# Performance work log

Hardware: AMD Instinct MI355X
Metric: run time of the kernel (lower is better)

The kernel has to match this reference:

```python
import jax, jax.numpy as jnp
import numpy as np

N_NODES = 50000
N_EDGES = 500000
F_IN = 16      # node feature dim F
F_OUT = 16     # channels F_
E_FEAT = 8     # edge feature dim
HIDDEN = 32    # kernel_network hidden size


def _glorot(key, shape):
    fan_in, fan_out = shape[0], shape[1]
    lim = np.sqrt(6.0 / (fan_in + fan_out)).astype(np.float32)
    return jax.random.uniform(key, shape, jnp.float32, -lim, lim)


def setup_inputs() -> dict:
    key = jax.random.key(0)
    ks = jax.random.split(key, 8)
    x = jax.random.normal(ks[0], (N_NODES, F_IN), jnp.float32)
    e = jax.random.uniform(ks[1], (N_EDGES, E_FEAT), jnp.float32)
    idx_i = jax.random.randint(ks[2], (N_EDGES,), 0, N_NODES, jnp.int32)  # targets
    idx_j = jax.random.randint(ks[3], (N_EDGES,), 0, N_NODES, jnp.int32)  # sources
    W1 = _glorot(ks[4], (E_FEAT, HIDDEN))
    b1 = jnp.zeros((HIDDEN,), jnp.float32)
    W2 = _glorot(ks[5], (HIDDEN, F_OUT * F_IN))
    b2 = jnp.zeros((F_OUT * F_IN,), jnp.float32)
    root_kernel = _glorot(ks[6], (F_IN, F_OUT))
    bias = jnp.zeros((F_OUT,), jnp.float32)
    return {"x": x, "e": e, "idx_i": idx_i, "idx_j": idx_j,
            "W1": W1, "b1": b1, "W2": W2, "b2": b2,
            "root_kernel": root_kernel, "bias": bias}


def reference(x, e, idx_i, idx_j, W1, b1, W2, b2, root_kernel, bias):
    # Edge-conditioned filter-generating network (MLP, relu hidden, linear out)
    h = jax.nn.relu(e @ W1 + b1)                       # [E, HIDDEN]
    kern = (h @ W2 + b2).reshape(-1, F_IN, F_OUT)      # [E, F, F_]
    # gather source node features, per-edge matmul, scatter-add to targets
    msg = jnp.einsum('ef,efc->ec', x[idx_j], kern)     # [E, F_]
    out = jax.ops.segment_sum(msg, idx_i, num_segments=N_NODES)  # [N, F_]
    out = out + x @ root_kernel + bias
    return out
```

## Files before the change

kernel.cpp:

```cpp
#include <hip/hip_runtime.h>

typedef __attribute__((ext_vector_type(8))) short bf16x8_t;
typedef __attribute__((ext_vector_type(4))) float f32x4_t;

__device__ __forceinline__ unsigned short f2bf(float f) {
    union { float f; unsigned int i; } v; v.f = f;
    unsigned int u = v.i;
    return (unsigned short)((u + 0x7FFFu + ((u >> 16) & 1u)) >> 16);
}

__device__ __forceinline__ unsigned int cvt_pk_bf16(float lo, float hi) {
    unsigned int r;
    asm("v_cvt_pk_bf16_f32 %0, %1, %2" : "=v"(r) : "v"(lo), "v"(hi));
    return r;
}

#define LD4(p) (*reinterpret_cast<const float4*>(p))


__global__ __launch_bounds__(256) void prep_kernel(
    const float* __restrict__ x,
    const float* __restrict__ W1,
    const float* __restrict__ b1,
    const float* __restrict__ W2,
    const float* __restrict__ b2,
    const float* __restrict__ rootk,
    const float* __restrict__ bias,
    float* __restrict__ out,
    unsigned short* __restrict__ tab,
    int n_nodes, int root_blocks)
{
    const int tid = threadIdx.x;
    const int bid = blockIdx.x;

    if (bid < root_blocks) {
        __shared__ float sR[256];
        __shared__ float sB[16];
        if (tid < 256) sR[tid] = rootk[tid];
        if (tid < 16)  sB[tid] = bias[tid];
        __syncthreads();

        int nid = bid * 256 + tid;
        if (nid >= n_nodes) return;

        const float* xp = x + (size_t)nid * 16;
        float xf[16];
#pragma unroll
        for (int f = 0; f < 16; f += 4) {
            float4 v = LD4(xp + f);
            xf[f] = v.x; xf[f + 1] = v.y; xf[f + 2] = v.z; xf[f + 3] = v.w;
        }
        float o[16];
#pragma unroll
        for (int cc = 0; cc < 16; ++cc) o[cc] = sB[cc];
#pragma unroll
        for (int f = 0; f < 16; ++f) {
            float p = xf[f];
#pragma unroll
            for (int cc = 0; cc < 16; ++cc)
                o[cc] = fmaf(p, sR[f * 16 + cc], o[cc]);
        }
        float* dst = out + (size_t)nid * 16;
#pragma unroll
        for (int cc = 0; cc < 16; cc += 4)
            *reinterpret_cast<float4*>(dst + cc) = make_float4(o[cc], o[cc+1], o[cc+2], o[cc+3]);
    } else {
        for (int it = tid; it < 64 * 19; it += 256) {
            int grp  = it >> 6;
            int lane = it & 63;
            int q = lane >> 4, cc = lane & 15;
            union { unsigned short h[8]; uint4 u; } pk;
            if (grp < 2) {
                int hh = grp;
#pragma unroll
                for (int j = 0; j < 8; ++j) {
                    float v = 0.f;
                    if (q == 0)              v = W1[j * 32 + cc + 16 * hh];
                    else if (q == 1 && j==0) v = b1[cc + 16 * hh];
                    pk.h[j] = f2bf(v);
                }
                *reinterpret_cast<uint4*>(tab + ((size_t)hh * 64 + lane) * 8) = pk.u;
            } else {
                int s = grp - 2;
#pragma unroll
                for (int j = 0; j < 8; ++j) {
                    float v;
                    if (s < 16) {
                        int hd = (j < 4) ? (4 * q + j) : (4 * q + 12 + j);
                        v = W2[hd * 256 + s * 16 + cc];
                    } else {
                        v = (q < 2) ? b2[(q * 8 + j) * 16 + cc] : 0.f;
                    }
                    pk.h[j] = f2bf(v);
                }
                *reinterpret_cast<uint4*>(tab + 1024 + ((size_t)s * 64 + lane) * 8) = pk.u;
            }
        }
    }
}

template<int EXACT>
__global__ __launch_bounds__(256) void edge_mfma_kernel(
    const float* __restrict__ x,
    const float* __restrict__ efeat,
    const int*   __restrict__ idx_i,
    const int*   __restrict__ idx_j,
    const unsigned short* __restrict__ tab,
    float* __restrict__ out,
    int n_edges, int n_groups)
{
    const int lane = threadIdx.x & 63;
    const int q = lane >> 4;
    const int c = lane & 15;

    const bf16x8_t* w1f = reinterpret_cast<const bf16x8_t*>(tab) + lane;
    const bf16x8_t aW1_0 = w1f[0];
    const bf16x8_t aW1_1 = w1f[64];
    const bf16x8_t* w2f = reinterpret_cast<const bf16x8_t*>(tab + 1024) + lane;
    bf16x8_t bW2[17];
#pragma unroll
    for (int s = 0; s < 17; ++s) bW2[s] = w2f[s * 64];

    const unsigned int c1 = (q == 1) ? 0x00003F80u : 0u;
    const bool isq0 = (q == 0);
    const bool qodd = (q & 1);
    float* const outc = out + c;

    const int wid = blockIdx.x * 4 + (threadIdx.x >> 6);
    const int g0  = wid * 4;
    if (g0 >= n_groups) return;
    const int rem = n_groups - g0;

    auto ldj = [&](int gg) -> int {
        int eid = gg * 16 + c;
        if (!EXACT) { if (eid >= n_edges) eid = n_edges - 1; }
        return idx_j[eid];
    };
    auto eoff = [&](int gg) -> size_t {
        int eid = gg * 16 + c;
        if (!EXACT) { if (eid >= n_edges) eid = n_edges - 1; }
        return (size_t)eid * 8;
    };

    auto compute = [&](float4 X0, float4 X1, float4 X2, float4 X3,
                       float4 E0, float4 E1, int gg) {
        int t0, t1, t2, t3;
        if (EXACT || (gg * 16 + 16 <= n_edges)) {
            int4 tv = *reinterpret_cast<const int4*>(idx_i + gg * 16 + q * 4);
            t0 = tv.x; t1 = tv.y; t2 = tv.z; t3 = tv.w;
        } else {
            const int eb = gg * 16 + q * 4;
            t0 = (eb + 0 < n_edges) ? idx_i[eb + 0] : 0;
            t1 = (eb + 1 < n_edges) ? idx_i[eb + 1] : 0;
            t2 = (eb + 2 < n_edges) ? idx_i[eb + 2] : 0;
            t3 = (eb + 3 < n_edges) ? idx_i[eb + 3] : 0;
        }

        union { bf16x8_t bf; unsigned int u[4]; } bB;
        {
            unsigned int ef0 = cvt_pk_bf16(E0.x, E0.y);
            unsigned int ef1 = cvt_pk_bf16(E0.z, E0.w);
            unsigned int ef2 = cvt_pk_bf16(E1.x, E1.y);
            unsigned int ef3 = cvt_pk_bf16(E1.z, E1.w);
            bB.u[0] = isq0 ? ef0 : c1;
            bB.u[1] = isq0 ? ef1 : 0u;
            bB.u[2] = isq0 ? ef2 : 0u;
            bB.u[3] = isq0 ? ef3 : 0u;
        }
        f32x4_t z4 = {0.f, 0.f, 0.f, 0.f};
        f32x4_t h0 = __builtin_amdgcn_mfma_f32_16x16x32_bf16(aW1_0, bB.bf, z4, 0, 0, 0);
        f32x4_t h1 = __builtin_amdgcn_mfma_f32_16x16x32_bf16(aW1_1, bB.bf, z4, 0, 0, 0);

        float hown[8];
#pragma unroll
        for (int r = 0; r < 4; ++r) {
            hown[r]     = fmaxf(h0[r], 0.f);
            hown[4 + r] = fmaxf(h1[r], 0.f);
        }

        float xf[16];
        xf[0]=X0.x; xf[1]=X0.y; xf[2]=X0.z; xf[3]=X0.w;
        xf[4]=X1.x; xf[5]=X1.y; xf[6]=X1.z; xf[7]=X1.w;
        xf[8]=X2.x; xf[9]=X2.y; xf[10]=X2.z; xf[11]=X2.w;
        xf[12]=X3.x; xf[13]=X3.y; xf[14]=X3.z; xf[15]=X3.w;

        union { bf16x8_t bf; unsigned int u[4]; } xb;
        xb.u[0] = cvt_pk_bf16(qodd ? xf[8]  : xf[0], qodd ? xf[9]  : xf[1]);
        xb.u[1] = cvt_pk_bf16(qodd ? xf[10] : xf[2], qodd ? xf[11] : xf[3]);
        xb.u[2] = cvt_pk_bf16(qodd ? xf[12] : xf[4], qodd ? xf[13] : xf[5]);
        xb.u[3] = cvt_pk_bf16(qodd ? xf[14] : xf[6], qodd ? xf[15] : xf[7]);

        f32x4_t acc0 = {0.f, 0.f, 0.f, 0.f};
        f32x4_t acc1 = {0.f, 0.f, 0.f, 0.f};
        union { bf16x8_t bf; unsigned int u[4]; } afr;
#pragma unroll
        for (int s = 0; s < 16; s += 2) {
            float xs = xf[s];
            afr.u[0] = cvt_pk_bf16(hown[0] * xs, hown[1] * xs);
            afr.u[1] = cvt_pk_bf16(hown[2] * xs, hown[3] * xs);
            afr.u[2] = cvt_pk_bf16(hown[4] * xs, hown[5] * xs);
            afr.u[3] = cvt_pk_bf16(hown[6] * xs, hown[7] * xs);
            acc0 = __builtin_amdgcn_mfma_f32_16x16x32_bf16(afr.bf, bW2[s], acc0, 0, 0, 0);
            xs = xf[s + 1];
            afr.u[0] = cvt_pk_bf16(hown[0] * xs, hown[1] * xs);
            afr.u[1] = cvt_pk_bf16(hown[2] * xs, hown[3] * xs);
            afr.u[2] = cvt_pk_bf16(hown[4] * xs, hown[5] * xs);
            afr.u[3] = cvt_pk_bf16(hown[6] * xs, hown[7] * xs);
            acc1 = __builtin_amdgcn_mfma_f32_16x16x32_bf16(afr.bf, bW2[s + 1], acc1, 0, 0, 0);
        }
        acc0 = __builtin_amdgcn_mfma_f32_16x16x32_bf16(xb.bf, bW2[16], acc0, 0, 0, 0);

        const float rr0 = acc0[0] + acc1[0];
        const float rr1 = acc0[1] + acc1[1];
        const float rr2 = acc0[2] + acc1[2];
        const float rr3 = acc0[3] + acc1[3];
        if (EXACT) {
            atomicAdd(outc + (size_t)t0 * 16, rr0);
            atomicAdd(outc + (size_t)t1 * 16, rr1);
            atomicAdd(outc + (size_t)t2 * 16, rr2);
            atomicAdd(outc + (size_t)t3 * 16, rr3);
        } else {
            const int eb = gg * 16 + q * 4;
            if (eb + 0 < n_edges) atomicAdd(outc + (size_t)t0 * 16, rr0);
            if (eb + 1 < n_edges) atomicAdd(outc + (size_t)t1 * 16, rr1);
            if (eb + 2 < n_edges) atomicAdd(outc + (size_t)t2 * 16, rr2);
            if (eb + 3 < n_edges) atomicAdd(outc + (size_t)t3 * 16, rr3);
        }
    };

#define STAGE(B0,B1,B2,B3,BE0,BE1, jv, gg)                         \
    {                                                              \
        const float* xp = x + (size_t)(jv) * 16;                   \
        B0 = LD4(xp); B1 = LD4(xp + 4);                            \
        B2 = LD4(xp + 8); B3 = LD4(xp + 12);                       \
        const float* ep = efeat + eoff(gg);                        \
        BE0 = LD4(ep); BE1 = LD4(ep + 4);                          \
    }

    const int jA = ldj(g0);
    const int jB = (rem > 1) ? ldj(g0 + 1) : 0;
    const int jC = (rem > 2) ? ldj(g0 + 2) : 0;
    const int jD = (rem > 3) ? ldj(g0 + 3) : 0;

    float4 a0, a1, a2, a3, ae0, ae1;
    float4 b0, b1, b2, b3, be0, be1;

    STAGE(a0,a1,a2,a3,ae0,ae1, jA, g0);
    if (rem > 1) STAGE(b0,b1,b2,b3,be0,be1, jB, g0 + 1);
    compute(a0,a1,a2,a3,ae0,ae1, g0);
    if (rem > 1) {
        if (rem > 2) STAGE(a0,a1,a2,a3,ae0,ae1, jC, g0 + 2);
        compute(b0,b1,b2,b3,be0,be1, g0 + 1);
        if (rem > 2) {
            if (rem > 3) STAGE(b0,b1,b2,b3,be0,be1, jD, g0 + 3);
            compute(a0,a1,a2,a3,ae0,ae1, g0 + 2);
            if (rem > 3) compute(b0,b1,b2,b3,be0,be1, g0 + 3);
        }
    }
#undef STAGE
}

extern "C" void kernel_launch(void* const* d_in, const int* in_sizes, int n_in,
                              void* d_out, int out_size, void* d_ws, size_t ws_size,
                              hipStream_t stream) {
    const float* x     = (const float*)d_in[0];
    const float* e     = (const float*)d_in[1];
    const int*   idx_i = (const int*)d_in[2];
    const int*   idx_j = (const int*)d_in[3];
    const float* W1    = (const float*)d_in[4];
    const float* b1    = (const float*)d_in[5];
    const float* W2    = (const float*)d_in[6];
    const float* b2    = (const float*)d_in[7];
    const float* rootk = (const float*)d_in[8];
    const float* bias  = (const float*)d_in[9];

    int n_nodes  = in_sizes[0] / 16;
    int n_edges  = in_sizes[2];
    int n_groups = (n_edges + 15) / 16;

    float* out = (float*)d_out;
    unsigned short* tab = (unsigned short*)d_ws;

    int root_blocks = (n_nodes + 255) / 256;
    prep_kernel<<<root_blocks + 1, 256, 0, stream>>>(x, W1, b1, W2, b2, rootk, bias,
                                                     out, tab, n_nodes, root_blocks);

    int blocks = (n_groups + 15) / 16;
    if ((n_edges & 15) == 0)
        edge_mfma_kernel<1><<<blocks, 256, 0, stream>>>(x, e, idx_i, idx_j, tab, out,
                                                        n_edges, n_groups);
    else
        edge_mfma_kernel<0><<<blocks, 256, 0, stream>>>(x, e, idx_i, idx_j, tab, out,
                                                        n_edges, n_groups);
}
```

Measured before the change: 44.23 us.

## Process eight edge groups per wave with triple-buffered gather prefetch

Each wave now handles eight 16-edge groups instead of four. All idx_j values are loaded up front, and a three-stage rotating register buffer keeps two gathers in flight while one group is computed. It also sets launch_bounds minimum occupancy to 2 and rewrites the hidden-times-x products as packed float2 multiplies so the compiler can emit packed FMA. The intent is to hide gather latency and amortise W2 register loading across more groups, at the cost of higher register pressure and fewer, larger waves.

```diff
diff --git a/kernel.cpp b/kernel.cpp
--- a/kernel.cpp
+++ b/kernel.cpp
@@ -2,6 +2,7 @@
 
 typedef __attribute__((ext_vector_type(8))) short bf16x8_t;
 typedef __attribute__((ext_vector_type(4))) float f32x4_t;
+typedef __attribute__((ext_vector_type(2))) float f32x2_t;
 
 __device__ __forceinline__ unsigned short f2bf(float f) {
     union { float f; unsigned int i; } v; v.f = f;
@@ -100,7 +101,7 @@
 }
 
 template<int EXACT>
-__global__ __launch_bounds__(256) void edge_mfma_kernel(
+__global__ __launch_bounds__(256, 2) void edge_mfma_kernel(
     const float* __restrict__ x,
     const float* __restrict__ efeat,
     const int*   __restrict__ idx_i,
@@ -127,19 +128,41 @@
     float* const outc = out + c;
 
     const int wid = blockIdx.x * 4 + (threadIdx.x >> 6);
-    const int g0  = wid * 4;
+    const int g0  = wid * 8;
     if (g0 >= n_groups) return;
     const int rem = n_groups - g0;
 
-    auto ldj = [&](int gg) -> int {
+    const int* jp = idx_j + (size_t)g0 * 16 + c;
+    int j0, j1, j2, j3, j4, j5, j6, j7;
+    if (EXACT) {
+        j0 = jp[0];
+        j1 = (rem > 1) ? jp[16]  : 0;
+        j2 = (rem > 2) ? jp[32]  : 0;
+        j3 = (rem > 3) ? jp[48]  : 0;
+        j4 = (rem > 4) ? jp[64]  : 0;
+        j5 = (rem > 5) ? jp[80]  : 0;
+        j6 = (rem > 6) ? jp[96]  : 0;
+        j7 = (rem > 7) ? jp[112] : 0;
+    } else {
+        auto ldj = [&](int k) -> int {
+            int eid = (g0 + k) * 16 + c;
+            if (eid >= n_edges) eid = n_edges - 1;
+            return idx_j[eid];
+        };
+        j0 = ldj(0);
+        j1 = (rem > 1) ? ldj(1) : 0;
+        j2 = (rem > 2) ? ldj(2) : 0;
+        j3 = (rem > 3) ? ldj(3) : 0;
+        j4 = (rem > 4) ? ldj(4) : 0;
+        j5 = (rem > 5) ? ldj(5) : 0;
+        j6 = (rem > 6) ? ldj(6) : 0;
+        j7 = (rem > 7) ? ldj(7) : 0;
+    }
+
+    auto eptr = [&](int gg) -> const float* {
         int eid = gg * 16 + c;
         if (!EXACT) { if (eid >= n_edges) eid = n_edges - 1; }
-        return idx_j[eid];
-    };
-    auto eoff = [&](int gg) -> size_t {
-        int eid = gg * 16 + c;
-        if (!EXACT) { if (eid >= n_edges) eid = n_edges - 1; }
-        return (size_t)eid * 8;
+        return efeat + (size_t)eid * 8;
     };
 
     auto compute = [&](float4 X0, float4 X1, float4 X2, float4 X3,
@@ -157,26 +180,20 @@
         }
 
         union { bf16x8_t bf; unsigned int u[4]; } bB;
-        {
-            unsigned int ef0 = cvt_pk_bf16(E0.x, E0.y);
-            unsigned int ef1 = cvt_pk_bf16(E0.z, E0.w);
-            unsigned int ef2 = cvt_pk_bf16(E1.x, E1.y);
-            unsigned int ef3 = cvt_pk_bf16(E1.z, E1.w);
-            bB.u[0] = isq0 ? ef0 : c1;
-            bB.u[1] = isq0 ? ef1 : 0u;
-            bB.u[2] = isq0 ? ef2 : 0u;
-            bB.u[3] = isq0 ? ef3 : 0u;
-        }
+        bB.u[0] = isq0 ? cvt_pk_bf16(E0.x, E0.y) : c1;
+        bB.u[1] = isq0 ? cvt_pk_bf16(E0.z, E0.w) : 0u;
+        bB.u[2] = isq0 ? cvt_pk_bf16(E1.x, E1.y) : 0u;
+        bB.u[3] = isq0 ? cvt_pk_bf16(E1.z, E1.w) : 0u;
+
         f32x4_t z4 = {0.f, 0.f, 0.f, 0.f};
         f32x4_t h0 = __builtin_amdgcn_mfma_f32_16x16x32_bf16(aW1_0, bB.bf, z4, 0, 0, 0);
         f32x4_t h1 = __builtin_amdgcn_mfma_f32_16x16x32_bf16(aW1_1, bB.bf, z4, 0, 0, 0);
 
-        float hown[8];
-#pragma unroll
-        for (int r = 0; r < 4; ++r) {
-            hown[r]     = fmaxf(h0[r], 0.f);
-            hown[4 + r] = fmaxf(h1[r], 0.f);
-        }
+        f32x2_t hp0, hp1, hp2, hp3;
+        hp0[0] = fmaxf(h0[0], 0.f); hp0[1] = fmaxf(h0[1], 0.f);
+        hp1[0] = fmaxf(h0[2], 0.f); hp1[1] = fmaxf(h0[3], 0.f);
+        hp2[0] = fmaxf(h1[0], 0.f); hp2[1] = fmaxf(h1[1], 0.f);
+        hp3[0] = fmaxf(h1[2], 0.f); hp3[1] = fmaxf(h1[3], 0.f);
 
         float xf[16];
         xf[0]=X0.x; xf[1]=X0.y; xf[2]=X0.z; xf[3]=X0.w;
@@ -195,17 +212,19 @@
         union { bf16x8_t bf; unsigned int u[4]; } afr;
 #pragma unroll
         for (int s = 0; s < 16; s += 2) {
-            float xs = xf[s];
-            afr.u[0] = cvt_pk_bf16(hown[0] * xs, hown[1] * xs);
-            afr.u[1] = cvt_pk_bf16(hown[2] * xs, hown[3] * xs);
-            afr.u[2] = cvt_pk_bf16(hown[4] * xs, hown[5] * xs);
-            afr.u[3] = cvt_pk_bf16(hown[6] * xs, hown[7] * xs);
+            f32x2_t xs2; xs2[0] = xf[s]; xs2[1] = xf[s];
+            f32x2_t p0 = hp0 * xs2, p1 = hp1 * xs2, p2 = hp2 * xs2, p3 = hp3 * xs2;
+            afr.u[0] = cvt_pk_bf16(p0[0], p0[1]);
+            afr.u[1] = cvt_pk_bf16(p1[0], p1[1]);
+            afr.u[2] = cvt_pk_bf16(p2[0], p2[1]);
+            afr.u[3] = cvt_pk_bf16(p3[0], p3[1]);
             acc0 = __builtin_amdgcn_mfma_f32_16x16x32_bf16(afr.bf, bW2[s], acc0, 0, 0, 0);
-            xs = xf[s + 1];
-            afr.u[0] = cvt_pk_bf16(hown[0] * xs, hown[1] * xs);
-            afr.u[1] = cvt_pk_bf16(hown[2] * xs, hown[3] * xs);
-            afr.u[2] = cvt_pk_bf16(hown[4] * xs, hown[5] * xs);
-            afr.u[3] = cvt_pk_bf16(hown[6] * xs, hown[7] * xs);
+            xs2[0] = xf[s + 1]; xs2[1] = xf[s + 1];
+            p0 = hp0 * xs2; p1 = hp1 * xs2; p2 = hp2 * xs2; p3 = hp3 * xs2;
+            afr.u[0] = cvt_pk_bf16(p0[0], p0[1]);
+            afr.u[1] = cvt_pk_bf16(p1[0], p1[1]);
+            afr.u[2] = cvt_pk_bf16(p2[0], p2[1]);
+            afr.u[3] = cvt_pk_bf16(p3[0], p3[1]);
             acc1 = __builtin_amdgcn_mfma_f32_16x16x32_bf16(afr.bf, bW2[s + 1], acc1, 0, 0, 0);
         }
         acc0 = __builtin_amdgcn_mfma_f32_16x16x32_bf16(xb.bf, bW2[16], acc0, 0, 0, 0);
@@ -233,30 +252,31 @@
         const float* xp = x + (size_t)(jv) * 16;                   \
         B0 = LD4(xp); B1 = LD4(xp + 4);                            \
         B2 = LD4(xp + 8); B3 = LD4(xp + 12);                       \
-        const float* ep = efeat + eoff(gg);                        \
+        const float* ep = eptr(gg);                                \
         BE0 = LD4(ep); BE1 = LD4(ep + 4);                          \
     }
 
-    const int jA = ldj(g0);
-    const int jB = (rem > 1) ? ldj(g0 + 1) : 0;
-    const int jC = (rem > 2) ? ldj(g0 + 2) : 0;
-    const int jD = (rem > 3) ? ldj(g0 + 3) : 0;
-
-    float4 a0, a1, a2, a3, ae0, ae1;
-    float4 b0, b1, b2, b3, be0, be1;
-
-    STAGE(a0,a1,a2,a3,ae0,ae1, jA, g0);
-    if (rem > 1) STAGE(b0,b1,b2,b3,be0,be1, jB, g0 + 1);
-    compute(a0,a1,a2,a3,ae0,ae1, g0);
-    if (rem > 1) {
-        if (rem > 2) STAGE(a0,a1,a2,a3,ae0,ae1, jC, g0 + 2);
-        compute(b0,b1,b2,b3,be0,be1, g0 + 1);
-        if (rem > 2) {
-            if (rem > 3) STAGE(b0,b1,b2,b3,be0,be1, jD, g0 + 3);
-            compute(a0,a1,a2,a3,ae0,ae1, g0 + 2);
-            if (rem > 3) compute(b0,b1,b2,b3,be0,be1, g0 + 3);
-        }
-    }
+    float4 Ax0, Ax1, Ax2, Ax3, Ae0, Ae1;
+    float4 Bx0, Bx1, Bx2, Bx3, Be0, Be1;
+    float4 Cx0, Cx1, Cx2, Cx3, Ce0, Ce1;
+
+    STAGE(Ax0,Ax1,Ax2,Ax3,Ae0,Ae1, j0, g0 + 0);
+    if (rem > 1) STAGE(Bx0,Bx1,Bx2,Bx3,Be0,Be1, j1, g0 + 1);
+    if (rem > 2) STAGE(Cx0,Cx1,Cx2,Cx3,Ce0,Ce1, j2, g0 + 2);
+
+    compute(Ax0,Ax1,Ax2,Ax3,Ae0,Ae1, g0 + 0);
+    if (rem > 3) STAGE(Ax0,Ax1,Ax2,Ax3,Ae0,Ae1, j3, g0 + 3);
+    if (rem > 1) compute(Bx0,Bx1,Bx2,Bx3,Be0,Be1, g0 + 1);
+    if (rem > 4) STAGE(Bx0,Bx1,Bx2,Bx3,Be0,Be1, j4, g0 + 4);
+    if (rem > 2) compute(Cx0,Cx1,Cx2,Cx3,Ce0,Ce1, g0 + 2);
+    if (rem > 5) STAGE(Cx0,Cx1,Cx2,Cx3,Ce0,Ce1, j5, g0 + 5);
+    if (rem > 3) compute(Ax0,Ax1,Ax2,Ax3,Ae0,Ae1, g0 + 3);
+    if (rem > 6) STAGE(Ax0,Ax1,Ax2,Ax3,Ae0,Ae1, j6, g0 + 6);
+    if (rem > 4) compute(Bx0,Bx1,Bx2,Bx3,Be0,Be1, g0 + 4);
+    if (rem > 7) STAGE(Bx0,Bx1,Bx2,Bx3,Be0,Be1, j7, g0 + 7);
+    if (rem > 5) compute(Cx0,Cx1,Cx2,Cx3,Ce0,Ce1, g0 + 5);
+    if (rem > 6) compute(Ax0,Ax1,Ax2,Ax3,Ae0,Ae1, g0 + 6);
+    if (rem > 7) compute(Bx0,Bx1,Bx2,Bx3,Be0,Be1, g0 + 7);
 #undef STAGE
 }
 
@@ -285,7 +305,8 @@
     prep_kernel<<<root_blocks + 1, 256, 0, stream>>>(x, W1, b1, W2, b2, rootk, bias,
                                                      out, tab, n_nodes, root_blocks);
 
-    int blocks = (n_groups + 15) / 16;
+    int waves  = (n_groups + 7) / 8;
+    int blocks = (waves + 3) / 4;
     if ((n_edges & 15) == 0)
         edge_mfma_kernel<1><<<blocks, 256, 0, stream>>>(x, e, idx_i, idx_j, tab, out,
                                                         n_edges, n_groups);
```

Measured after the change: 47.83 us. 8.1% more time.

## Switch edge MFMA path to fp16 with packed multiplies and shuffle-shared x gathers

Applied to the files above, without the earlier changes.

Moves the weight table and MFMA inputs from bf16 to fp16. This lets the per-source-feature scaling of the hidden activations use packed half-precision multiplies instead of fp32 multiplies followed by bf16 conversions. Each lane now loads only a quarter of the gathered x row, and the wave reassembles full rows with cross-lane shuffles, cutting redundant gather loads by four. The trade-offs are fp16 range and precision limits, since round-toward-zero conversion and fp16 products may reduce accuracy, and the added shuffle instructions.

```diff
diff --git a/kernel.cpp b/kernel.cpp
--- a/kernel.cpp
+++ b/kernel.cpp
@@ -1,18 +1,14 @@
 #include <hip/hip_runtime.h>
 
-typedef __attribute__((ext_vector_type(8))) short bf16x8_t;
+typedef __attribute__((ext_vector_type(8))) _Float16 f16x8_t;
+typedef __attribute__((ext_vector_type(2))) _Float16 f16x2_t;
 typedef __attribute__((ext_vector_type(4))) float f32x4_t;
 
-__device__ __forceinline__ unsigned short f2bf(float f) {
-    union { float f; unsigned int i; } v; v.f = f;
-    unsigned int u = v.i;
-    return (unsigned short)((u + 0x7FFFu + ((u >> 16) & 1u)) >> 16);
-}
-
-__device__ __forceinline__ unsigned int cvt_pk_bf16(float lo, float hi) {
-    unsigned int r;
-    asm("v_cvt_pk_bf16_f32 %0, %1, %2" : "=v"(r) : "v"(lo), "v"(hi));
-    return r;
+__device__ __forceinline__ f16x2_t pkh(float lo, float hi) {
+    return __builtin_bit_cast(f16x2_t, __builtin_amdgcn_cvt_pkrtz(lo, hi));
+}
+__device__ __forceinline__ unsigned int pkrtz(float lo, float hi) {
+    return __builtin_bit_cast(unsigned int, __builtin_amdgcn_cvt_pkrtz(lo, hi));
 }
 
 #define LD4(p) (*reinterpret_cast<const float4*>(p))
@@ -27,7 +23,7 @@
     const float* __restrict__ rootk,
     const float* __restrict__ bias,
     float* __restrict__ out,
-    unsigned short* __restrict__ tab,
+    _Float16* __restrict__ tab,
     int n_nodes, int root_blocks)
 {
     const int tid = threadIdx.x;
@@ -69,7 +65,7 @@
             int grp  = it >> 6;
             int lane = it & 63;
             int q = lane >> 4, cc = lane & 15;
-            union { unsigned short h[8]; uint4 u; } pk;
+            union { _Float16 h[8]; uint4 u; } pk;
             if (grp < 2) {
                 int hh = grp;
 #pragma unroll
@@ -77,7 +73,7 @@
                     float v = 0.f;
                     if (q == 0)              v = W1[j * 32 + cc + 16 * hh];
                     else if (q == 1 && j==0) v = b1[cc + 16 * hh];
-                    pk.h[j] = f2bf(v);
+                    pk.h[j] = (_Float16)v;
                 }
                 *reinterpret_cast<uint4*>(tab + ((size_t)hh * 64 + lane) * 8) = pk.u;
             } else {
@@ -91,12 +87,19 @@
                     } else {
                         v = (q < 2) ? b2[(q * 8 + j) * 16 + cc] : 0.f;
                     }
-                    pk.h[j] = f2bf(v);
+                    pk.h[j] = (_Float16)v;
                 }
                 *reinterpret_cast<uint4*>(tab + 1024 + ((size_t)s * 64 + lane) * 8) = pk.u;
             }
         }
     }
+}
+
+__device__ __forceinline__ float4 shfl4(float4 v, int src) {
+    float4 r;
+    r.x = __shfl(v.x, src); r.y = __shfl(v.y, src);
+    r.z = __shfl(v.z, src); r.w = __shfl(v.w, src);
+    return r;
 }
 
 template<int EXACT>
@@ -105,7 +108,7 @@
     const float* __restrict__ efeat,
     const int*   __restrict__ idx_i,
     const int*   __restrict__ idx_j,
-    const unsigned short* __restrict__ tab,
+    const _Float16* __restrict__ tab,
     float* __restrict__ out,
     int n_edges, int n_groups)
 {
@@ -113,15 +116,15 @@
     const int q = lane >> 4;
     const int c = lane & 15;
 
-    const bf16x8_t* w1f = reinterpret_cast<const bf16x8_t*>(tab) + lane;
-    const bf16x8_t aW1_0 = w1f[0];
-    const bf16x8_t aW1_1 = w1f[64];
-    const bf16x8_t* w2f = reinterpret_cast<const bf16x8_t*>(tab + 1024) + lane;
-    bf16x8_t bW2[17];
+    const f16x8_t* w1f = reinterpret_cast<const f16x8_t*>(tab) + lane;
+    const f16x8_t aW1_0 = w1f[0];
+    const f16x8_t aW1_1 = w1f[64];
+    const f16x8_t* w2f = reinterpret_cast<const f16x8_t*>(tab + 1024) + lane;
+    f16x8_t bW2[17];
 #pragma unroll
     for (int s = 0; s < 17; ++s) bW2[s] = w2f[s * 64];
 
-    const unsigned int c1 = (q == 1) ? 0x00003F80u : 0u;
+    const unsigned int c1 = (q == 1) ? 0x00003C00u : 0u;
     const bool isq0 = (q == 0);
     const bool qodd = (q & 1);
     float* const outc = out + c;
@@ -136,14 +139,13 @@
         if (!EXACT) { if (eid >= n_edges) eid = n_edges - 1; }
         return idx_j[eid];
     };
-    auto eoff = [&](int gg) -> size_t {
+    auto eptr = [&](int gg) -> const float* {
         int eid = gg * 16 + c;
         if (!EXACT) { if (eid >= n_edges) eid = n_edges - 1; }
-        return (size_t)eid * 8;
+        return efeat + (size_t)eid * 8;
     };
 
-    auto compute = [&](float4 X0, float4 X1, float4 X2, float4 X3,
-                       float4 E0, float4 E1, int gg) {
+    auto compute = [&](float4 XQ, float4 E0, float4 E1, int gg) {
         int t0, t1, t2, t3;
         if (EXACT || (gg * 16 + 16 <= n_edges)) {
             int4 tv = *reinterpret_cast<const int4*>(idx_i + gg * 16 + q * 4);
@@ -156,27 +158,25 @@
             t3 = (eb + 3 < n_edges) ? idx_i[eb + 3] : 0;
         }
 
-        union { bf16x8_t bf; unsigned int u[4]; } bB;
-        {
-            unsigned int ef0 = cvt_pk_bf16(E0.x, E0.y);
-            unsigned int ef1 = cvt_pk_bf16(E0.z, E0.w);
-            unsigned int ef2 = cvt_pk_bf16(E1.x, E1.y);
-            unsigned int ef3 = cvt_pk_bf16(E1.z, E1.w);
-            bB.u[0] = isq0 ? ef0 : c1;
-            bB.u[1] = isq0 ? ef1 : 0u;
-            bB.u[2] = isq0 ? ef2 : 0u;
-            bB.u[3] = isq0 ? ef3 : 0u;
-        }
+        float4 X0 = shfl4(XQ, c);
+        float4 X1 = shfl4(XQ, c + 16);
+        float4 X2 = shfl4(XQ, c + 32);
+        float4 X3 = shfl4(XQ, c + 48);
+
+        union { f16x8_t v8; f16x2_t v2[4]; unsigned int u[4]; } bB;
+        bB.u[0] = isq0 ? pkrtz(E0.x, E0.y) : c1;
+        bB.u[1] = isq0 ? pkrtz(E0.z, E0.w) : 0u;
+        bB.u[2] = isq0 ? pkrtz(E1.x, E1.y) : 0u;
+        bB.u[3] = isq0 ? pkrtz(E1.z, E1.w) : 0u;
+
         f32x4_t z4 = {0.f, 0.f, 0.f, 0.f};
-        f32x4_t h0 = __builtin_amdgcn_mfma_f32_16x16x32_bf16(aW1_0, bB.bf, z4, 0, 0, 0);
-        f32x4_t h1 = __builtin_amdgcn_mfma_f32_16x16x32_bf16(aW1_1, bB.bf, z4, 0, 0, 0);
-
-        float hown[8];
-#pragma unroll
-        for (int r = 0; r < 4; ++r) {
-            hown[r]     = fmaxf(h0[r], 0.f);
-            hown[4 + r] = fmaxf(h1[r], 0.f);
-        }
+        f32x4_t h0 = __builtin_amdgcn_mfma_f32_16x16x32_f16(aW1_0, bB.v8, z4, 0, 0, 0);
+        f32x4_t h1 = __builtin_amdgcn_mfma_f32_16x16x32_f16(aW1_1, bB.v8, z4, 0, 0, 0);
+
+        f16x2_t hp0 = pkh(fmaxf(h0[0], 0.f), fmaxf(h0[1], 0.f));
+        f16x2_t hp1 = pkh(fmaxf(h0[2], 0.f), fmaxf(h0[3], 0.f));
+        f16x2_t hp2 = pkh(fmaxf(h1[0], 0.f), fmaxf(h1[1], 0.f));
+        f16x2_t hp3 = pkh(fmaxf(h1[2], 0.f), fmaxf(h1[3], 0.f));
 
         float xf[16];
         xf[0]=X0.x; xf[1]=X0.y; xf[2]=X0.z; xf[3]=X0.w;
@@ -184,31 +184,36 @@
         xf[8]=X2.x; xf[9]=X2.y; xf[10]=X2.z; xf[11]=X2.w;
         xf[12]=X3.x; xf[13]=X3.y; xf[14]=X3.z; xf[15]=X3.w;
 
-        union { bf16x8_t bf; unsigned int u[4]; } xb;
-        xb.u[0] = cvt_pk_bf16(qodd ? xf[8]  : xf[0], qodd ? xf[9]  : xf[1]);
-        xb.u[1] = cvt_pk_bf16(qodd ? xf[10] : xf[2], qodd ? xf[11] : xf[3]);
-        xb.u[2] = cvt_pk_bf16(qodd ? xf[12] : xf[4], qodd ? xf[13] : xf[5]);
-        xb.u[3] = cvt_pk_bf16(qodd ? xf[14] : xf[6], qodd ? xf[15] : xf[7]);
+        f16x2_t xss[16];
+#pragma unroll
+        for (int f = 0; f < 16; ++f)
+            xss[f] = pkh(xf[f], xf[f]);
+
+        union { f16x8_t v8; unsigned int u[4]; } xb;
+        xb.u[0] = pkrtz(qodd ? xf[8]  : xf[0], qodd ? xf[9]  : xf[1]);
+        xb.u[1] = pkrtz(qodd ? xf[10] : xf[2], qodd ? xf[11] : xf[3]);
+        xb.u[2] = pkrtz(qodd ? xf[12] : xf[4], qodd ? xf[13] : xf[5]);
+        xb.u[3] = pkrtz(qodd ? xf[14] : xf[6], qodd ? xf[15] : xf[7]);
 
         f32x4_t acc0 = {0.f, 0.f, 0.f, 0.f};
         f32x4_t acc1 = {0.f, 0.f, 0.f, 0.f};
-        union { bf16x8_t bf; unsigned int u[4]; } afr;
+        union { f16x8_t v8; f16x2_t v2[4]; } afr;
 #pragma unroll
         for (int s = 0; s < 16; s += 2) {
-            float xs = xf[s];
-            afr.u[0] = cvt_pk_bf16(hown[0] * xs, hown[1] * xs);
-            afr.u[1] = cvt_pk_bf16(hown[2] * xs, hown[3] * xs);
-            afr.u[2] = cvt_pk_bf16(hown[4] * xs, hown[5] * xs);
-            afr.u[3] = cvt_pk_bf16(hown[6] * xs, hown[7] * xs);
-            acc0 = __builtin_amdgcn_mfma_f32_16x16x32_bf16(afr.bf, bW2[s], acc0, 0, 0, 0);
-            xs = xf[s + 1];
-            afr.u[0] = cvt_pk_bf16(hown[0] * xs, hown[1] * xs);
-            afr.u[1] = cvt_pk_bf16(hown[2] * xs, hown[3] * xs);
-            afr.u[2] = cvt_pk_bf16(hown[4] * xs, hown[5] * xs);
-            afr.u[3] = cvt_pk_bf16(hown[6] * xs, hown[7] * xs);
-            acc1 = __builtin_amdgcn_mfma_f32_16x16x32_bf16(afr.bf, bW2[s + 1], acc1, 0, 0, 0);
-        }
-        acc0 = __builtin_amdgcn_mfma_f32_16x16x32_bf16(xb.bf, bW2[16], acc0, 0, 0, 0);
+            f16x2_t xs2 = xss[s];
+            afr.v2[0] = hp0 * xs2;
+            afr.v2[1] = hp1 * xs2;
+            afr.v2[2] = hp2 * xs2;
+            afr.v2[3] = hp3 * xs2;
+            acc0 = __builtin_amdgcn_mfma_f32_16x16x32_f16(afr.v8, bW2[s], acc0, 0, 0, 0);
+            xs2 = xss[s + 1];
+            afr.v2[0] = hp0 * xs2;
+            afr.v2[1] = hp1 * xs2;
+            afr.v2[2] = hp2 * xs2;
+            afr.v2[3] = hp3 * xs2;
+            acc1 = __builtin_amdgcn_mfma_f32_16x16x32_f16(afr.v8, bW2[s + 1], acc1, 0, 0, 0);
+        }
+        acc0 = __builtin_amdgcn_mfma_f32_16x16x32_f16(xb.v8, bW2[16], acc0, 0, 0, 0);
 
         const float rr0 = acc0[0] + acc1[0];
         const float rr1 = acc0[1] + acc1[1];
@@ -228,13 +233,11 @@
         }
     };
 
-#define STAGE(B0,B1,B2,B3,BE0,BE1, jv, gg)                         \
-    {                                                              \
-        const float* xp = x + (size_t)(jv) * 16;                   \
-        B0 = LD4(xp); B1 = LD4(xp + 4);                            \
-        B2 = LD4(xp + 8); B3 = LD4(xp + 12);                       \
-        const float* ep = efeat + eoff(gg);                        \
-        BE0 = LD4(ep); BE1 = LD4(ep + 4);                          \
+#define STAGE(BXQ, BE0, BE1, jv, gg)                                \
+    {                                                               \
+        BXQ = LD4(x + (size_t)(jv) * 16 + q * 4);                   \
+        const float* ep = eptr(gg);                                 \
+        BE0 = LD4(ep); BE1 = LD4(ep + 4);                           \
     }
 
     const int jA = ldj(g0);
@@ -242,19 +245,19 @@
     const int jC = (rem > 2) ? ldj(g0 + 2) : 0;
     const int jD = (rem > 3) ? ldj(g0 + 3) : 0;
 
-    float4 a0, a1, a2, a3, ae0, ae1;
-    float4 b0, b1, b2, b3, be0, be1;
-
-    STAGE(a0,a1,a2,a3,ae0,ae1, jA, g0);
-    if (rem > 1) STAGE(b0,b1,b2,b3,be0,be1, jB, g0 + 1);
-    compute(a0,a1,a2,a3,ae0,ae1, g0);
+    float4 aq, ae0, ae1;
+    float4 bq, be0, be1;
+
+    STAGE(aq, ae0, ae1, jA, g0);
+    if (rem > 1) STAGE(bq, be0, be1, jB, g0 + 1);
+    compute(aq, ae0, ae1, g0);
     if (rem > 1) {
-        if (rem > 2) STAGE(a0,a1,a2,a3,ae0,ae1, jC, g0 + 2);
-        compute(b0,b1,b2,b3,be0,be1, g0 + 1);
+        if (rem > 2) STAGE(aq, ae0, ae1, jC, g0 + 2);
+        compute(bq, be0, be1, g0 + 1);
         if (rem > 2) {
-            if (rem > 3) STAGE(b0,b1,b2,b3,be0,be1, jD, g0 + 3);
-            compute(a0,a1,a2,a3,ae0,ae1, g0 + 2);
-            if (rem > 3) compute(b0,b1,b2,b3,be0,be1, g0 + 3);
+            if (rem > 3) STAGE(bq, be0, be1, jD, g0 + 3);
+            compute(aq, ae0, ae1, g0 + 2);
+            if (rem > 3) compute(bq, be0, be1, g0 + 3);
         }
     }
 #undef STAGE
@@ -279,7 +282,7 @@
     int n_groups = (n_edges + 15) / 16;
 
     float* out = (float*)d_out;
-    unsigned short* tab = (unsigned short*)d_ws;
+    _Float16* tab = (_Float16*)d_ws;
 
     int root_blocks = (n_nodes + 255) / 256;
     prep_kernel<<<root_blocks + 1, 256, 0, stream>>>(x, W1, b1, W2, b2, rootk, bias,
```

Measured after the change: 46.22 us. 1.05x slower.
